# Performance work log

Hardware: AMD Instinct MI355X
Metric: run time of the kernel (lower is better)

The kernel has to match this reference:

```python
import jax, jax.numpy as jnp
import numpy as np

N_NODES = 50000
TAU = 1.0 + (1.0 / 1000.0) * (0.1 - 1.0)  # anneal step 1 -> 0.9991


def setup_inputs() -> dict:
    key = jax.random.key(0)
    ks = jax.random.split(key, 8)
    N, F, H, E, K = N_NODES, 128, 128, 800000, 5
    node_features = jax.random.normal(ks[0], (N, F), dtype=jnp.float32)
    src = jnp.sort(jax.random.randint(ks[1], (E,), 0, N, dtype=jnp.int32))
    dst = jax.random.randint(ks[2], (E,), 0, N, dtype=jnp.int32)
    u_noise = jax.random.uniform(ks[3], (K, E), dtype=jnp.float32,
                                 minval=1e-6, maxval=1.0 - 1e-6)
    # MLP params: Linear(2F -> H), ReLU, Linear(H -> 1)
    W1 = jax.random.normal(ks[4], (2 * F, H), dtype=jnp.float32) / np.sqrt(2 * F)
    b1 = jnp.zeros((H,), dtype=jnp.float32)
    W2 = jax.random.normal(ks[5], (H, 1), dtype=jnp.float32) / np.sqrt(H)
    b2 = jnp.zeros((1,), dtype=jnp.float32)
    return {"node_features": node_features, "W1": W1, "b1": b1,
            "W2": W2, "b2": b2, "u_noise": u_noise, "src": src, "dst": dst}


def reference(node_features, W1, b1, W2, b2, u_noise, src, dst):
    N = N_NODES
    F = node_features.shape[1]
    # per-edge MLP on concat([x_u, x_v]) without materializing the (E, 2F) concat
    x_u = node_features[src]                      # (E, F)
    x_v = node_features[dst]                      # (E, F)
    h = jax.nn.relu(x_u @ W1[:F] + x_v @ W1[F:] + b1)   # (E, H)
    z = (h @ W2 + b2)[:, 0]                       # (E,)
    # per-node (segment) log-softmax over each node's neighbor edges
    zmax = jax.ops.segment_max(z, src, num_segments=N)
    ze = z - zmax[src]
    denom = jax.ops.segment_sum(jnp.exp(ze), src, num_segments=N)
    log_pi = ze - jnp.log(denom)[src]             # (E,)
    # k rounds of Gumbel-softmax sampling
    g = -jnp.log(-jnp.log(u_noise))               # (K, E)
    scores = (log_pi[None, :] + g) / TAU          # (K, E)

    def seg_softmax(s):
        m = jax.ops.segment_max(s, src, num_segments=N)
        e = jnp.exp(s - m[src])
        return e / jax.ops.segment_sum(e, src, num_segments=N)[src]

    def seg_argmax_dst(s):
        m = jax.ops.segment_max(s, src, num_segments=N)
        hit = s >= m[src]
        sel = jax.ops.segment_max(jnp.where(hit, dst, -1), src, num_segments=N)
        return sel  # (N,) selected neighbor per node, per round

    soft = jax.vmap(seg_softmax)(scores)          # (K, E) gumbel-softmax probs
    selected = jax.vmap(seg_argmax_dst)(scores)   # (K, N) sampled neighbor ids
    return selected, soft
```

## Files before the change

### kernel.cpp

```cpp
#include <hip/hip_runtime.h>

#define FEAT 128
#define HID  128
#define XS_S 132

__global__ __launch_bounds__(256) void gemm_ab(
    const float* __restrict__ X, const float* __restrict__ W1,
    const float* __restrict__ b1, float* __restrict__ A,
    float* __restrict__ B, int N) {
  __shared__ float xs[32 * XS_S];
  const int t = threadIdx.x;

  const int nb = gridDim.x;
  const int q = nb >> 3, r = nb & 7;
  const int xcd = blockIdx.x & 7, bidx = blockIdx.x >> 3;
  const int nw = (xcd < r ? xcd * (q + 1) : r * (q + 1) + (xcd - r) * q) + bidx;
  const int n0 = (nw >> 2) * 128;
  const int jb = (nw & 3) * 64;
  const int isA = jb < 128;
  const int ob = jb & 127;
  const float* Wb = W1 + (size_t)(isA ? 0 : 128 * HID) + ob;
  float* Obase = isA ? A : B;

  const int l = t & 63;
  const int wv16 = __builtin_amdgcn_readfirstlane((t >> 6) * 16);
  const float* Wp = Wb + wv16;

  float acc0[16], acc1[16];
#pragma unroll
  for (int c = 0; c < 16; ++c) { acc0[c] = 0.f; acc1[c] = 0.f; }

  const int ln = t >> 3;
  const int lf = (t & 7) * 4;

  for (int kc = 0; kc < 4; ++kc) {
    __syncthreads();
#pragma unroll
    for (int rep = 0; rep < 4; ++rep) {
      const int nl = ln + rep * 32;
      const int n = n0 + nl;
      float4 v = make_float4(0.f, 0.f, 0.f, 0.f);
      if (n < N) v = *(const float4*)(X + (size_t)n * FEAT + kc * 32 + lf);
      xs[(lf + 0) * XS_S + nl] = v.x;
      xs[(lf + 1) * XS_S + nl] = v.y;
      xs[(lf + 2) * XS_S + nl] = v.z;
      xs[(lf + 3) * XS_S + nl] = v.w;
    }
    __syncthreads();

#pragma unroll 4
    for (int k = 0; k < 32; ++k) {
      const float2 xv = *(const float2*)&xs[k * XS_S + 2 * l];
      const float* wr = Wp + (size_t)(kc * 32 + k) * HID;
      float wv[16];
      *(float4*)&wv[0]  = *(const float4*)(wr);
      *(float4*)&wv[4]  = *(const float4*)(wr + 4);
      *(float4*)&wv[8]  = *(const float4*)(wr + 8);
      *(float4*)&wv[12] = *(const float4*)(wr + 12);
#pragma unroll
      for (int c = 0; c < 16; ++c) {
        acc0[c] = fmaf(xv.x, wv[c], acc0[c]);
        acc1[c] = fmaf(xv.y, wv[c], acc1[c]);
      }
    }
  }

  float4 bb[4];
#pragma unroll
  for (int c = 0; c < 4; ++c) bb[c] = make_float4(0.f, 0.f, 0.f, 0.f);
  if (isA) {
#pragma unroll
    for (int c = 0; c < 4; ++c)
      bb[c] = *(const float4*)(b1 + ob + wv16 + c * 4);
  }
  const int na = n0 + 2 * l;
  const int nbb = na + 1;
  if (na < N) {
    float* o = Obase + (size_t)na * HID + ob + wv16;
#pragma unroll
    for (int c = 0; c < 4; ++c)
      *(float4*)(o + c * 4) = make_float4(
          acc0[c * 4 + 0] + bb[c].x, acc0[c * 4 + 1] + bb[c].y,
          acc0[c * 4 + 2] + bb[c].z, acc0[c * 4 + 3] + bb[c].w);
  }
  if (nbb < N) {
    float* o = Obase + (size_t)nbb * HID + ob + wv16;
#pragma unroll
    for (int c = 0; c < 4; ++c)
      *(float4*)(o + c * 4) = make_float4(
          acc1[c * 4 + 0] + bb[c].x, acc1[c * 4 + 1] + bb[c].y,
          acc1[c * 4 + 2] + bb[c].z, acc1[c * 4 + 3] + bb[c].w);
  }
}

__global__ __launch_bounds__(256) void row_offsets(
    const int* __restrict__ src, int* __restrict__ rs, int N, int E) {
  const int n = blockIdx.x * 256 + threadIdx.x;
  if (n > N) return;
  int lo = 0, hi = E;
  while (lo < hi) {
    const int mid = (lo + hi) >> 1;
    if (src[mid] < n) lo = mid + 1; else hi = mid;
  }
  rs[n] = lo;
}

__global__ __launch_bounds__(256) void edge_z(
    const float* __restrict__ A, const float* __restrict__ B,
    const float* __restrict__ W2, const float* __restrict__ b2,
    const int* __restrict__ src, const int* __restrict__ dst,
    float* __restrict__ z, int E) {
  const int g = threadIdx.x >> 4;
  const int l = threadIdx.x & 15;
  const int e0 = blockIdx.x * 32 + g * 2;
  if (e0 >= E) return;
  const int e1 = e0 + 1;
  const bool has1 = e1 < E;

  const int u0 = src[e0], v0 = dst[e0];
  const int u1 = has1 ? src[e1] : u0;
  const int v1 = has1 ? dst[e1] : v0;

  const float4* Au0 = (const float4*)(A + (size_t)u0 * HID) + l * 2;
  const float4* Bv0 = (const float4*)(B + (size_t)v0 * HID) + l * 2;
  const float4* Au1 = (const float4*)(A + (size_t)u1 * HID) + l * 2;
  const float4* Bv1 = (const float4*)(B + (size_t)v1 * HID) + l * 2;

  const float4 a00 = Au0[0], a01 = Au0[1];
  const float4 b00 = Bv0[0], b01 = Bv0[1];
  const float4 a10 = Au1[0], a11 = Au1[1];
  const float4 b10 = Bv1[0], b11 = Bv1[1];

  const float4 w0 = *(const float4*)(W2 + l * 8);
  const float4 w1 = *(const float4*)(W2 + l * 8 + 4);
  const float bias2 = b2[0];

  float p0 = fmaxf(a00.x + b00.x, 0.f) * w0.x
           + fmaxf(a00.y + b00.y, 0.f) * w0.y
           + fmaxf(a00.z + b00.z, 0.f) * w0.z
           + fmaxf(a00.w + b00.w, 0.f) * w0.w
           + fmaxf(a01.x + b01.x, 0.f) * w1.x
           + fmaxf(a01.y + b01.y, 0.f) * w1.y
           + fmaxf(a01.z + b01.z, 0.f) * w1.z
           + fmaxf(a01.w + b01.w, 0.f) * w1.w;
  float p1 = fmaxf(a10.x + b10.x, 0.f) * w0.x
           + fmaxf(a10.y + b10.y, 0.f) * w0.y
           + fmaxf(a10.z + b10.z, 0.f) * w0.z
           + fmaxf(a10.w + b10.w, 0.f) * w0.w
           + fmaxf(a11.x + b11.x, 0.f) * w1.x
           + fmaxf(a11.y + b11.y, 0.f) * w1.y
           + fmaxf(a11.z + b11.z, 0.f) * w1.z
           + fmaxf(a11.w + b11.w, 0.f) * w1.w;

#pragma unroll
  for (int m = 8; m >= 1; m >>= 1) {
    p0 += __shfl_xor(p0, m);
    p1 += __shfl_xor(p1, m);
  }
  if (l == 0) {
    z[e0] = p0 + bias2;
    if (has1) z[e1] = p1 + bias2;
  }
}

__global__ __launch_bounds__(256) void seg_sample(
    const float* __restrict__ z, const float* __restrict__ U,
    const int* __restrict__ dst, const int* __restrict__ rs,
    float* __restrict__ out_sel, float* __restrict__ out_soft,
    int N, int E, int K) {
  const int t = threadIdx.x;
  const int lane = t & 63;
  const int qtr = lane >> 4;
  const int ql = lane & 15;
  const int n = blockIdx.x * 16 + (t >> 6) * 4 + qtr;
  const float INVTAU = 1.0f / 0.9991f;

  int start = 0, deg = 0;
  if (n < N) { start = rs[n]; deg = rs[n + 1] - start; }

  if (__all(deg <= 32)) {
    if (n >= N) return;
    if (deg == 0) {
      if (ql == 0)
        for (int k = 0; k < K; ++k) out_sel[(size_t)k * N + n] = -2147483648.0f;
      return;
    }
    const bool a0 = 2 * ql < deg;
    const bool a1 = 2 * ql + 1 < deg;
    const int e0 = start + 2 * ql;
    const int e1 = e0 + 1;
    const float z0 = a0 ? z[e0] : -INFINITY;
    const float z1 = a1 ? z[e1] : -INFINITY;
    const int d0 = a0 ? dst[e0] : -1;
    const int d1 = a1 ? dst[e1] : -1;

    float zmax = fmaxf(z0, z1);
#pragma unroll
    for (int m = 8; m >= 1; m >>= 1) zmax = fmaxf(zmax, __shfl_xor(zmax, m));
    float den = (a0 ? __expf(z0 - zmax) : 0.f) + (a1 ? __expf(z1 - zmax) : 0.f);
#pragma unroll
    for (int m = 8; m >= 1; m >>= 1) den += __shfl_xor(den, m);
    const float logd = __logf(den);
    const float lp0 = (z0 - zmax) - logd;
    const float lp1 = (z1 - zmax) - logd;

    for (int k = 0; k < K; ++k) {
      float ex0 = 0.f, ex1 = 0.f;
      if (a0) {
        const float uu = U[(size_t)k * E + e0];
        const float gum = -__logf(-__logf(uu));
        ex0 = __expf((lp0 + gum) * INVTAU);
      }
      if (a1) {
        const float uu = U[(size_t)k * E + e1];
        const float gum = -__logf(-__logf(uu));
        ex1 = __expf((lp1 + gum) * INVTAU);
      }
      float d2 = ex0 + ex1;
      float mx;
      int md;
      if (ex1 > ex0)      { mx = ex1; md = d1; }
      else if (ex1 < ex0) { mx = ex0; md = d0; }
      else                { mx = ex0; md = max(d0, d1); }
#pragma unroll
      for (int m = 8; m >= 1; m >>= 1) {
        d2 += __shfl_xor(d2, m);
        const float ox = __shfl_xor(mx, m);
        const int od = __shfl_xor(md, m);
        if (ox > mx) { mx = ox; md = od; }
        else if (ox == mx) md = max(md, od);
      }
      if (ql == 0) out_sel[(size_t)k * N + n] = (float)md;
      const float inv = __builtin_amdgcn_rcpf(d2);
      if (a0) out_soft[(size_t)k * E + e0] = ex0 * inv;
      if (a1) out_soft[(size_t)k * E + e1] = ex1 * inv;
    }
    return;
  }

  const int wbase = blockIdx.x * 16 + (t >> 6) * 4;
  for (int j = 0; j < 4; ++j) {
    const int nn = wbase + j;
    if (nn >= N) continue;
    const int st = rs[nn];
    const int dg = rs[nn + 1] - st;
    if (dg == 0) {
      if (lane == 0)
        for (int k = 0; k < K; ++k) out_sel[(size_t)k * N + nn] = -2147483648.0f;
      continue;
    }
    float zmax = -INFINITY;
    for (int c = lane; c < dg; c += 64) zmax = fmaxf(zmax, z[st + c]);
#pragma unroll
    for (int m = 32; m >= 1; m >>= 1) zmax = fmaxf(zmax, __shfl_xor(zmax, m));
    float den = 0.f;
    for (int c = lane; c < dg; c += 64) den += expf(z[st + c] - zmax);
#pragma unroll
    for (int m = 32; m >= 1; m >>= 1) den += __shfl_xor(den, m);
    const float logd = logf(den);

    for (int k = 0; k < K; ++k) {
      float m2 = -INFINITY;
      for (int c = lane; c < dg; c += 64) {
        const int e = st + c;
        const float gum = -logf(-logf(U[(size_t)k * E + e]));
        const float s = ((z[e] - zmax) - logd + gum) * INVTAU;
        m2 = fmaxf(m2, s);
      }
#pragma unroll
      for (int m = 32; m >= 1; m >>= 1) m2 = fmaxf(m2, __shfl_xor(m2, m));
      float d2 = 0.f;
      int cand = -1;
      for (int c = lane; c < dg; c += 64) {
        const int e = st + c;
        const float gum = -logf(-logf(U[(size_t)k * E + e]));
        const float s = ((z[e] - zmax) - logd + gum) * INVTAU;
        d2 += expf(s - m2);
        if (s >= m2) cand = max(cand, dst[e]);
      }
#pragma unroll
      for (int m = 32; m >= 1; m >>= 1) d2 += __shfl_xor(d2, m);
#pragma unroll
      for (int m = 32; m >= 1; m >>= 1) cand = max(cand, __shfl_xor(cand, m));
      if (lane == 0) out_sel[(size_t)k * N + nn] = (float)cand;
      for (int c = lane; c < dg; c += 64) {
        const int e = st + c;
        const float gum = -logf(-logf(U[(size_t)k * E + e]));
        const float s = ((z[e] - zmax) - logd + gum) * INVTAU;
        out_soft[(size_t)k * E + e] = expf(s - m2) / d2;
      }
    }
  }
}

extern "C" void kernel_launch(void* const* d_in, const int* in_sizes, int n_in,
                              void* d_out, int out_size, void* d_ws, size_t ws_size,
                              hipStream_t stream) {
  const float* X  = (const float*)d_in[0];
  const float* W1 = (const float*)d_in[1];
  const float* b1 = (const float*)d_in[2];
  const float* W2 = (const float*)d_in[3];
  const float* b2 = (const float*)d_in[4];
  const float* U  = (const float*)d_in[5];
  const int* src  = (const int*)d_in[6];
  const int* dst  = (const int*)d_in[7];
  const int E = in_sizes[6];
  const int K = in_sizes[5] / E;
  const int N = in_sizes[0] / FEAT;

  float* A = (float*)d_ws;
  float* B = A + (size_t)N * HID;
  float* z = B + (size_t)N * HID;
  int* rs  = (int*)(z + E);

  float* out_sel  = (float*)d_out;
  float* out_soft = (float*)d_out + (size_t)K * N;

  hipLaunchKernelGGL(gemm_ab, dim3(4 * ((N + 127) / 128)), dim3(256), 0, stream,
                     X, W1, b1, A, B, N);
  hipLaunchKernelGGL(row_offsets, dim3((N + 256) / 256), dim3(256), 0, stream,
                     src, rs, N, E);
  hipLaunchKernelGGL(edge_z, dim3((E + 31) / 32), dim3(256), 0, stream,
                     A, B, W2, b2, src, dst, z, E);
  hipLaunchKernelGGL(seg_sample, dim3((N + 15) / 16), dim3(256), 0, stream,
                     z, U, dst, rs, out_sel, out_soft, N, E, K);
}
```

Baseline: 246.2 us.

## Retile node-feature GEMM to one node per lane with 32-column register tiles

Restructures the gemm_ab kernel so each block handles 64 nodes and a full 128-column half (A or B). Each lane owns one node and 32 output columns, keeping 32 X values per K-chunk in registers. X is now stored row-major in shared memory with padding, and wave-uniform W1 rows are read in pairs. The aim is more FMA work per W load and fewer shared-memory reads. The cost is higher register pressure (32 accumulators plus 64 weight values), which may lower occupancy.

```diff
diff --git a/kernel.cpp b/kernel.cpp
--- a/kernel.cpp
+++ b/kernel.cpp
@@ -2,94 +2,85 @@
 
 #define FEAT 128
 #define HID  128
-#define XS_S 132
+#define XT_S 33
 
 __global__ __launch_bounds__(256) void gemm_ab(
     const float* __restrict__ X, const float* __restrict__ W1,
     const float* __restrict__ b1, float* __restrict__ A,
     float* __restrict__ B, int N) {
-  __shared__ float xs[32 * XS_S];
+  __shared__ float xs[64 * XT_S];
   const int t = threadIdx.x;
 
   const int nb = gridDim.x;
   const int q = nb >> 3, r = nb & 7;
   const int xcd = blockIdx.x & 7, bidx = blockIdx.x >> 3;
   const int nw = (xcd < r ? xcd * (q + 1) : r * (q + 1) + (xcd - r) * q) + bidx;
-  const int n0 = (nw >> 2) * 128;
-  const int jb = (nw & 3) * 64;
-  const int isA = jb < 128;
-  const int ob = jb & 127;
-  const float* Wb = W1 + (size_t)(isA ? 0 : 128 * HID) + ob;
+  const int n0 = (nw >> 1) * 64;
+  const int isA = (nw & 1) == 0;
+  const float* Wb = W1 + (isA ? 0 : (size_t)128 * HID);
   float* Obase = isA ? A : B;
 
   const int l = t & 63;
-  const int wv16 = __builtin_amdgcn_readfirstlane((t >> 6) * 16);
-  const float* Wp = Wb + wv16;
-
-  float acc0[16], acc1[16];
-#pragma unroll
-  for (int c = 0; c < 16; ++c) { acc0[c] = 0.f; acc1[c] = 0.f; }
-
-  const int ln = t >> 3;
-  const int lf = (t & 7) * 4;
+  const int cb = __builtin_amdgcn_readfirstlane((t >> 6) * 32);
+
+  float acc[32];
+#pragma unroll
+  for (int c = 0; c < 32; ++c) acc[c] = 0.f;
 
   for (int kc = 0; kc < 4; ++kc) {
     __syncthreads();
 #pragma unroll
-    for (int rep = 0; rep < 4; ++rep) {
-      const int nl = ln + rep * 32;
+    for (int rep = 0; rep < 2; ++rep) {
+      const int idx = rep * 256 + t;
+      const int nl = idx >> 3;
+      const int qd = (idx & 7) * 4;
       const int n = n0 + nl;
       float4 v = make_float4(0.f, 0.f, 0.f, 0.f);
-      if (n < N) v = *(const float4*)(X + (size_t)n * FEAT + kc * 32 + lf);
-      xs[(lf + 0) * XS_S + nl] = v.x;
-      xs[(lf + 1) * XS_S + nl] = v.y;
-      xs[(lf + 2) * XS_S + nl] = v.z;
-      xs[(lf + 3) * XS_S + nl] = v.w;
+      if (n < N) v = *(const float4*)(X + (size_t)n * FEAT + kc * 32 + qd);
+      xs[nl * XT_S + qd + 0] = v.x;
+      xs[nl * XT_S + qd + 1] = v.y;
+      xs[nl * XT_S + qd + 2] = v.z;
+      xs[nl * XT_S + qd + 3] = v.w;
     }
     __syncthreads();
 
-#pragma unroll 4
-    for (int k = 0; k < 32; ++k) {
-      const float2 xv = *(const float2*)&xs[k * XS_S + 2 * l];
-      const float* wr = Wp + (size_t)(kc * 32 + k) * HID;
-      float wv[16];
-      *(float4*)&wv[0]  = *(const float4*)(wr);
-      *(float4*)&wv[4]  = *(const float4*)(wr + 4);
-      *(float4*)&wv[8]  = *(const float4*)(wr + 8);
-      *(float4*)&wv[12] = *(const float4*)(wr + 12);
-#pragma unroll
-      for (int c = 0; c < 16; ++c) {
-        acc0[c] = fmaf(xv.x, wv[c], acc0[c]);
-        acc1[c] = fmaf(xv.y, wv[c], acc1[c]);
-      }
-    }
-  }
-
-  float4 bb[4];
-#pragma unroll
-  for (int c = 0; c < 4; ++c) bb[c] = make_float4(0.f, 0.f, 0.f, 0.f);
+    float xr[32];
+#pragma unroll
+    for (int j = 0; j < 32; ++j) xr[j] = xs[l * XT_S + j];
+
+#pragma unroll
+    for (int k = 0; k < 32; k += 2) {
+      const float* w0p = Wb + (size_t)(kc * 32 + k) * HID + cb;
+      const float* w1p = w0p + HID;
+      float wv0[32], wv1[32];
+#pragma unroll
+      for (int c4 = 0; c4 < 8; ++c4) {
+        *(float4*)&wv0[c4 * 4] = *(const float4*)(w0p + c4 * 4);
+        *(float4*)&wv1[c4 * 4] = *(const float4*)(w1p + c4 * 4);
+      }
+#pragma unroll
+      for (int c = 0; c < 32; ++c) acc[c] = fmaf(xr[k], wv0[c], acc[c]);
+#pragma unroll
+      for (int c = 0; c < 32; ++c) acc[c] = fmaf(xr[k + 1], wv1[c], acc[c]);
+    }
+  }
+
+  float bb[32];
+#pragma unroll
+  for (int c = 0; c < 32; ++c) bb[c] = 0.f;
   if (isA) {
 #pragma unroll
-    for (int c = 0; c < 4; ++c)
-      bb[c] = *(const float4*)(b1 + ob + wv16 + c * 4);
-  }
-  const int na = n0 + 2 * l;
-  const int nbb = na + 1;
-  if (na < N) {
-    float* o = Obase + (size_t)na * HID + ob + wv16;
-#pragma unroll
-    for (int c = 0; c < 4; ++c)
-      *(float4*)(o + c * 4) = make_float4(
-          acc0[c * 4 + 0] + bb[c].x, acc0[c * 4 + 1] + bb[c].y,
-          acc0[c * 4 + 2] + bb[c].z, acc0[c * 4 + 3] + bb[c].w);
-  }
-  if (nbb < N) {
-    float* o = Obase + (size_t)nbb * HID + ob + wv16;
-#pragma unroll
-    for (int c = 0; c < 4; ++c)
-      *(float4*)(o + c * 4) = make_float4(
-          acc1[c * 4 + 0] + bb[c].x, acc1[c * 4 + 1] + bb[c].y,
-          acc1[c * 4 + 2] + bb[c].z, acc1[c * 4 + 3] + bb[c].w);
+    for (int c4 = 0; c4 < 8; ++c4)
+      *(float4*)&bb[c4 * 4] = *(const float4*)(b1 + cb + c4 * 4);
+  }
+  const int n = n0 + l;
+  if (n < N) {
+    float* o = Obase + (size_t)n * HID + cb;
+#pragma unroll
+    for (int c4 = 0; c4 < 8; ++c4)
+      *(float4*)(o + c4 * 4) = make_float4(
+          acc[c4 * 4 + 0] + bb[c4 * 4 + 0], acc[c4 * 4 + 1] + bb[c4 * 4 + 1],
+          acc[c4 * 4 + 2] + bb[c4 * 4 + 2], acc[c4 * 4 + 3] + bb[c4 * 4 + 3]);
   }
 }
 
@@ -316,7 +307,7 @@
   float* out_sel  = (float*)d_out;
   float* out_soft = (float*)d_out + (size_t)K * N;
 
-  hipLaunchKernelGGL(gemm_ab, dim3(4 * ((N + 127) / 128)), dim3(256), 0, stream,
+  hipLaunchKernelGGL(gemm_ab, dim3(2 * ((N + 63) / 64)), dim3(256), 0, stream,
                      X, W1, b1, A, B, N);
   hipLaunchKernelGGL(row_offsets, dim3((N + 256) / 256), dim3(256), 0, stream,
                      src, rs, N, E);
```

After: 257.4 us. +4.5%, slower.
